# Kernel tuning notes

Measured on AMD Instinct MI355X. Metric: run time of the kernel, lower is better.

Reference implementation:

```python
import jax, jax.numpy as jnp
import numpy as np
from itertools import product

D = 64          # dense grid extent per axis
B = 2           # batch size
N_PER = 65536
NF_IN = 3
NF = 32
EPS = 1e-5


def _ravel(c):
    # c: [Q,4] (b,x,y,z) -> unique linear key
    return ((c[:, 0] * D + c[:, 1]) * D + c[:, 2]) * D + c[:, 3]


def _build_indices():
    """Build active coords and rule-book index tables (numpy, host-side)."""
    rng = np.random.default_rng(0)
    parts = []
    for b in range(B):
        lin = rng.choice(D ** 3, size=N_PER, replace=False)
        x = lin // (D * D)
        y = (lin // D) % D
        z = lin % D
        parts.append(np.stack([np.full(N_PER, b), x, y, z], 1))
    coords = np.concatenate(parts, 0).astype(np.int64)  # [N,4]
    keys = _ravel(coords)
    order = np.argsort(keys)
    skeys = keys[order]

    def lookup(qc):
        valid = ((qc[:, 1:] >= 0) & (qc[:, 1:] < D)).all(1)
        qc2 = np.where(valid[:, None], qc, 0)
        qk = _ravel(qc2)
        pos = np.clip(np.searchsorted(skeys, qk), 0, len(skeys) - 1)
        found = valid & (skeys[pos] == qk)
        return np.where(found, order[pos], -1)

    # 3x3x3 submanifold rule-book: neighbor index per active site per offset
    offs3 = list(product((-1, 0, 1), repeat=3))
    nbr = np.stack([lookup(coords + np.array([0, dx, dy, dz]))
                    for dx, dy, dz in offs3], 1)  # [N,27]
    # 2x2x2 stride-2 conv: output sites = unique parent cells
    parents = np.unique(np.concatenate([coords[:, :1], coords[:, 1:] // 2], 1), axis=0)
    base = parents * np.array([1, 2, 2, 2])
    offs2 = list(product((0, 1), repeat=3))
    child = np.stack([lookup(base + np.array([0, dx, dy, dz]))
                      for dx, dy, dz in offs2], 1)  # [M,8]
    return nbr.astype(np.int32), child.astype(np.int32)


def setup_inputs() -> dict:
    nbr, child = _build_indices()
    N = nbr.shape[0]
    key = jax.random.key(0)
    ks = jax.random.split(key, 6)

    def w(k, shape, fan):
        return jax.random.normal(k, shape, jnp.float32) / np.float32(np.sqrt(fan))

    ones = jnp.ones((NF,), jnp.float32)
    zeros = jnp.zeros((NF,), jnp.float32)
    return {
        "feats": jax.random.normal(ks[0], (N, NF_IN), jnp.float32),
        "nbr_idx": jnp.asarray(nbr),
        "child_idx": jnp.asarray(child),
        "W1": w(ks[1], (27, NF_IN, NF), 27 * NF_IN),
        "W2a": w(ks[2], (27, NF, NF), 27 * NF),
        "W2b": w(ks[3], (27, NF, NF), 27 * NF),
        "W3": w(ks[4], (8, NF, NF), 8 * NF),
        "g1": ones, "b1": zeros,
        "g2": ones, "b2": zeros,
        "g3": ones, "b3": zeros,
        "g4": ones, "b4": zeros,
    }


def _gconv(feats, idx, W):
    # sparse conv as rule-book gather -> per-offset GEMM -> accumulate
    mask = (idx >= 0)
    g = feats[jnp.clip(idx, 0)] * mask[..., None].astype(feats.dtype)  # [N,K,C]
    return jnp.einsum('nkc,kcd->nd', g, W)


def _bnrelu(x, g, b):
    # training-mode BN over active sites, then ReLU (scn.BatchNormReLU)
    mu = x.mean(0)
    var = x.var(0)
    return jax.nn.relu((x - mu) * jax.lax.rsqrt(var + EPS) * g + b)


def reference(feats, nbr_idx, child_idx, W1, W2a, W2b, W3,
              g1, b1, g2, b2, g3, b3, g4, b4):
    x1 = _gconv(feats, nbr_idx, W1)                       # p1: submanifold 3^3
    br = _gconv(_bnrelu(x1, g1, b1), nbr_idx, W2a)        # p2 residual branch
    br = _gconv(_bnrelu(br, g2, b2), nbr_idx, W2b)
    ft2 = _bnrelu(x1 + br, g3, b3)                        # AddTable + BNReLU
    x3 = _gconv(ft2, child_idx, W3)                       # p3: 2^3 stride-2 conv
    out = _bnrelu(x3, g4, b4)
    return (out, ft2)
```

## Files before the change

kernel.cpp:

```cpp
#include <hip/hip_runtime.h>
#include <hip/hip_bf16.h>


typedef __bf16 bf16_8 __attribute__((ext_vector_type(8)));
typedef float  f32x4  __attribute__((ext_vector_type(4)));

#define EPSV 1e-5f
#define NCOPY 32
#define CBLK 256

__global__ __launch_bounds__(256) void k_cnt(const int* __restrict__ child, int m8,
                                             int* __restrict__ blockCnt) {
    __shared__ int ws[4];
    const int b = blockIdx.x, tid = threadIdx.x;
    const int chunk = (m8 + CBLK - 1) / CBLK;
    const int s0 = b * chunk, s1 = min(s0 + chunk, m8);
    int c = 0;
    for (int s = s0 + tid; s < s1; s += 256) c += (child[s] >= 0);
#pragma unroll
    for (int d = 1; d < 64; d <<= 1) c += __shfl_xor(c, d);
    if ((tid & 63) == 0) ws[tid >> 6] = c;
    __syncthreads();
    if (tid == 0) blockCnt[b] = ws[0] + ws[1] + ws[2] + ws[3];
}

__global__ __launch_bounds__(256) void k_compact(const int* __restrict__ child, int m8,
                                                 const int* __restrict__ blockCnt,
                                                 int* __restrict__ perm,
                                                 int* __restrict__ invperm) {
    __shared__ int woff[4];
    __shared__ int sbase;
    const int b = blockIdx.x, tid = threadIdx.x;
    const int chunk = (m8 + CBLK - 1) / CBLK;
    const int s0 = b * chunk, s1 = min(s0 + chunk, m8);
    if (tid == 0) {
        int a = 0;
        for (int i = 0; i < b; ++i) a += blockCnt[i];
        sbase = a;
    }
    __syncthreads();
    int off = sbase;
    for (int base = s0; base < s1; base += 256) {
        const int s = base + tid;
        int c = -1;
        bool v = false;
        if (s < s1) { c = child[s]; v = (c >= 0); }
        unsigned long long m = __ballot(v);
        if ((tid & 63) == 0) woff[tid >> 6] = __popcll(m);
        __syncthreads();
        const int wv = tid >> 6;
        int wpre = 0;
#pragma unroll
        for (int i = 0; i < 4; ++i) if (i < wv) wpre += woff[i];
        const int tot = woff[0] + woff[1] + woff[2] + woff[3];
        const int rank = __popcll(m & ((1ULL << (tid & 63)) - 1ULL));
        if (v) {
            const int pos = off + wpre + rank;
            perm[pos] = c;
            invperm[c] = pos;
        }
        off += tot;
        __syncthreads();
    }
}

__global__ __launch_bounds__(256) void k_reindex(
    const int* __restrict__ nbr, const int* __restrict__ child,
    const int* __restrict__ perm, const int* __restrict__ invperm,
    const float* __restrict__ feats,
    const float* __restrict__ W1, const float* __restrict__ W2a,
    const float* __restrict__ W2b, const float* __restrict__ W3,
    int* __restrict__ nbrT, int* __restrict__ childT,
    __bf16* __restrict__ X, __bf16* __restrict__ T, __bf16* __restrict__ FB,
    __bf16* __restrict__ w1t, __bf16* __restrict__ w2at,
    __bf16* __restrict__ w2bt, __bf16* __restrict__ w3t,
    float* __restrict__ statsAll,
    int N, int M, int MP) {
    int t = blockIdx.x * 256 + threadIdx.x;
    if (t < 28 * N) {
        const int k = t / N, p = t - k * N;
        int o = N;
        if (k < 27) {
            const int v = nbr[(size_t)perm[p] * 27 + k];
            o = (v < 0) ? N : invperm[v];
        }
        nbrT[t] = o;
        return;
    }
    t -= 28 * N;
    if (t < 8 * MP) {
        const int k = t / MP, m = t - k * MP;
        int o = N;
        if (m < M) {
            const int v = child[(size_t)m * 8 + k];
            o = (v < 0) ? N : invperm[v];
        }
        childT[t] = o;
        return;
    }
    t -= 8 * MP;
    if (t < N * 32) {
        const int p = t >> 5, c = t & 31;
        FB[t] = (c < 3) ? (__bf16)feats[(size_t)perm[p] * 3 + c] : (__bf16)0.f;
        return;
    }
    t -= N * 32;
    if (t < 96) {
        const int b = t >> 5, c = t & 31;
        __bf16* p = (b == 0) ? X : (b == 1) ? T : FB;
        p[(size_t)N * 32 + c] = (__bf16)0.f;
        return;
    }
    t -= 96;
    if (t < 28672) {
        const int k = t >> 10, r = t & 1023, d = r >> 5, c = r & 31;
        w1t[t] = (k < 27 && c < 3) ? (__bf16)W1[(k * 3 + c) * 32 + d] : (__bf16)0.f;
        return;
    }
    t -= 28672;
    if (t < 28672) {
        const int k = t >> 10, r = t & 1023, d = r >> 5, c = r & 31;
        w2at[t] = (k < 27) ? (__bf16)W2a[(k * 32 + c) * 32 + d] : (__bf16)0.f;
        return;
    }
    t -= 28672;
    if (t < 28672) {
        const int k = t >> 10, r = t & 1023, d = r >> 5, c = r & 31;
        w2bt[t] = (k < 27) ? (__bf16)W2b[(k * 32 + c) * 32 + d] : (__bf16)0.f;
        return;
    }
    t -= 28672;
    if (t < 8192) {
        const int k = t >> 10, r = t & 1023, d = r >> 5, c = r & 31;
        w3t[t] = (__bf16)W3[(k * 32 + c) * 32 + d];
        return;
    }
    t -= 8192;
    if (t < 4 * NCOPY * 64) statsAll[t] = 0.f;
}

template <int KOFF, bool ADD>
__global__ __launch_bounds__(256, 4) void k_conv(
    const __bf16* __restrict__ src,
    const int* __restrict__ idxT,
    const __bf16* __restrict__ Wt,
    const __bf16* __restrict__ addsrc,
    __bf16* __restrict__ dst,
    float* __restrict__ spart_out,
    int nout, int npad) {
    constexpr int KPAD = ((KOFF + 3) / 4) * 4;
    constexpr int KPW = KPAD / 4;
    __shared__ float part[4][32][34];
    __shared__ float lst[64];

    const int tid = threadIdx.x;
    const int lane = tid & 63;
    const int wv = tid >> 6;
    const int base = blockIdx.x * 32;
    const int sl = lane & 15;
    const int kh = lane >> 4;
    const int kbeg = wv * KPW;

    if (tid < 64) lst[tid] = 0.f;

    int nb[2][KPW];
#pragma unroll
    for (int j = 0; j < KPW; ++j)
#pragma unroll
        for (int g = 0; g < 2; ++g)
            nb[g][j] = idxT[(kbeg + j) * npad + base + g * 16 + sl];

    bf16_8 av[2][KPW];
#pragma unroll
    for (int j = 0; j < KPW; ++j)
#pragma unroll
        for (int g = 0; g < 2; ++g)
            av[g][j] = *(const bf16_8*)(src + (size_t)nb[g][j] * 32 + kh * 8);
    __builtin_amdgcn_sched_barrier(0);

    f32x4 acc[2][2];
#pragma unroll
    for (int g = 0; g < 2; ++g)
#pragma unroll
        for (int h = 0; h < 2; ++h)
#pragma unroll
            for (int r = 0; r < 4; ++r) acc[g][h][r] = 0.f;

#pragma unroll
    for (int j = 0; j < KPW; ++j) {
        const int kk = kbeg + j;
        bf16_8 b0 = *(const bf16_8*)(Wt + kk * 1024 + sl * 32 + kh * 8);
        bf16_8 b1 = *(const bf16_8*)(Wt + kk * 1024 + (16 + sl) * 32 + kh * 8);
        acc[0][0] = __builtin_amdgcn_mfma_f32_16x16x32_bf16(av[0][j], b0, acc[0][0], 0, 0, 0);
        acc[0][1] = __builtin_amdgcn_mfma_f32_16x16x32_bf16(av[0][j], b1, acc[0][1], 0, 0, 0);
        acc[1][0] = __builtin_amdgcn_mfma_f32_16x16x32_bf16(av[1][j], b0, acc[1][0], 0, 0, 0);
        acc[1][1] = __builtin_amdgcn_mfma_f32_16x16x32_bf16(av[1][j], b1, acc[1][1], 0, 0, 0);
    }

#pragma unroll
    for (int g = 0; g < 2; ++g)
#pragma unroll
        for (int h = 0; h < 2; ++h)
#pragma unroll
            for (int r = 0; r < 4; ++r)
                part[wv][g * 16 + kh * 4 + r][h * 16 + sl] = acc[g][h][r];
    __syncthreads();

    if (tid < 128) {
        const int sloc = tid >> 2;
        const int c0 = (tid & 3) * 8;
        float v[8];
#pragma unroll
        for (int i = 0; i < 8; ++i)
            v[i] = part[0][sloc][c0 + i] + part[1][sloc][c0 + i] +
                   part[2][sloc][c0 + i] + part[3][sloc][c0 + i];
        const int site = base + sloc;
        if (site < nout) {
            if (ADD) {
                bf16_8 ad = *(const bf16_8*)(addsrc + (size_t)site * 32 + c0);
#pragma unroll
                for (int i = 0; i < 8; ++i) v[i] += (float)ad[i];
            }
            bf16_8 o;
#pragma unroll
            for (int i = 0; i < 8; ++i) o[i] = (__bf16)v[i];
            *(bf16_8*)(dst + (size_t)site * 32 + c0) = o;
        } else {
#pragma unroll
            for (int i = 0; i < 8; ++i) v[i] = 0.f;
        }
        float sv[8], qv[8];
#pragma unroll
        for (int i = 0; i < 8; ++i) { sv[i] = v[i]; qv[i] = v[i] * v[i]; }
#pragma unroll
        for (int d = 4; d < 64; d <<= 1) {
#pragma unroll
            for (int i = 0; i < 8; ++i) {
                sv[i] += __shfl_xor(sv[i], d);
                qv[i] += __shfl_xor(qv[i], d);
            }
        }
        if ((lane & 60) == 0) {
#pragma unroll
            for (int i = 0; i < 8; ++i) {
                atomicAdd(&lst[c0 + i], sv[i]);
                atomicAdd(&lst[32 + c0 + i], qv[i]);
            }
        }
    }
    __syncthreads();
    if (tid < 64)
        atomicAdd(&spart_out[(blockIdx.x & (NCOPY - 1)) * 64 + tid], lst[tid]);
}

template <bool WF32, bool WBF>
__global__ __launch_bounds__(256) void k_bn(
    const __bf16* __restrict__ src, const float* __restrict__ spart,
    const float* __restrict__ gamma, const float* __restrict__ beta,
    float inv_cnt, int nrows,
    __bf16* __restrict__ dstb, float* __restrict__ dstf,
    const int* __restrict__ permw) {
    __shared__ float ss[64];
    __shared__ float sc[32], sh[32];
    const int tid = threadIdx.x;
    if (tid < 64) {
        float a = 0.f;
#pragma unroll
        for (int i = 0; i < NCOPY; ++i) a += spart[i * 64 + tid];
        ss[tid] = a;
    }
    __syncthreads();
    if (tid < 32) {
        float mu = ss[tid] * inv_cnt;
        float var = ss[32 + tid] * inv_cnt - mu * mu;
        float s = gamma[tid] * rsqrtf(var + EPSV);
        sc[tid] = s;
        sh[tid] = beta[tid] - mu * s;
    }
    __syncthreads();
    const int gtid = blockIdx.x * blockDim.x + tid;
    const int c0 = (gtid & 3) * 8;
    float scale[8], shift[8];
#pragma unroll
    for (int i = 0; i < 8; ++i) { scale[i] = sc[c0 + i]; shift[i] = sh[c0 + i]; }
    const int rstride = (gridDim.x * blockDim.x) >> 2;
    for (int r = gtid >> 2; r < nrows; r += rstride) {
        const size_t off = (size_t)r * 32 + c0;
        bf16_8 v = *(const bf16_8*)(src + off);
        float y[8];
#pragma unroll
        for (int i = 0; i < 8; ++i) y[i] = fmaxf(fmaf((float)v[i], scale[i], shift[i]), 0.f);
        if (WBF) {
            bf16_8 o;
#pragma unroll
            for (int i = 0; i < 8; ++i) o[i] = (__bf16)y[i];
            *(bf16_8*)(dstb + off) = o;
        }
        if (WF32) {
            f32x4 lo, hi;
#pragma unroll
            for (int i = 0; i < 4; ++i) { lo[i] = y[i]; hi[i] = y[4 + i]; }
            const size_t woff = permw ? ((size_t)permw[r] * 32 + c0) : off;
            *(f32x4*)(dstf + woff) = lo;
            *(f32x4*)(dstf + woff + 4) = hi;
        }
    }
}

extern "C" void kernel_launch(void* const* d_in, const int* in_sizes, int n_in,
                              void* d_out, int out_size, void* d_ws, size_t ws_size,
                              hipStream_t stream) {
    const float* feats = (const float*)d_in[0];
    const int* nbr     = (const int*)d_in[1];
    const int* child   = (const int*)d_in[2];
    const float* W1  = (const float*)d_in[3];
    const float* W2a = (const float*)d_in[4];
    const float* W2b = (const float*)d_in[5];
    const float* W3  = (const float*)d_in[6];
    const float* g1 = (const float*)d_in[7];  const float* b1 = (const float*)d_in[8];
    const float* g2 = (const float*)d_in[9];  const float* b2 = (const float*)d_in[10];
    const float* g3 = (const float*)d_in[11]; const float* b3 = (const float*)d_in[12];
    const float* g4 = (const float*)d_in[13]; const float* b4 = (const float*)d_in[14];

    const int N = in_sizes[0] / 3;
    const int M8 = in_sizes[2];
    const int M = M8 / 8;
    const int MP = ((M + 31) / 32) * 32;

    float* outp = (float*)d_out;
    float* ft2p = outp + (size_t)M * 32;

    char* ws = (char*)d_ws;
    float* statsAll = (float*)ws;
    __bf16* w1t  = (__bf16*)(ws + 32768);
    __bf16* w2at = w1t + 28672;
    __bf16* w2bt = w2at + 28672;
    __bf16* w3t  = w2bt + 28672;
    __bf16* X  = (__bf16*)(ws + 221184);
    __bf16* T  = X + (size_t)(N + 1) * 32;
    __bf16* FB = T + (size_t)(N + 1) * 32;
    char* p2 = (char*)(FB + (size_t)(N + 1) * 32);
    int* perm    = (int*)p2;
    int* invperm = perm + N;
    int* nbrT    = invperm + N;
    int* childT  = nbrT + (size_t)28 * N;
    int* blockCnt = childT + (size_t)8 * MP;

    float* s1 = statsAll;
    float* s2 = statsAll + NCOPY * 64;
    float* s3 = statsAll + 2 * NCOPY * 64;
    float* s4 = statsAll + 3 * NCOPY * 64;

    k_cnt<<<CBLK, 256, 0, stream>>>(child, M8, blockCnt);
    k_compact<<<CBLK, 256, 0, stream>>>(child, M8, blockCnt, perm, invperm);

    const int rtot = 28 * N + 8 * MP + N * 32 + 96 + 3 * 28672 + 8192 + 4 * NCOPY * 64;
    k_reindex<<<(rtot + 255) / 256, 256, 0, stream>>>(
        nbr, child, perm, invperm, feats, W1, W2a, W2b, W3,
        nbrT, childT, X, T, FB, w1t, w2at, w2bt, w3t, statsAll, N, M, MP);

    const int cgrid = N / 32;
    const int cgrid3 = MP / 32;
    const float invN = 1.f / N, invM = 1.f / M;

    k_conv<27, false><<<cgrid, 256, 0, stream>>>(FB, nbrT, w1t, nullptr, X, s1, N, N);
    k_bn<false, true><<<1024, 256, 0, stream>>>(X, s1, g1, b1, invN, N, T, nullptr, nullptr);
    k_conv<27, false><<<cgrid, 256, 0, stream>>>(T, nbrT, w2at, nullptr, FB, s2, N, N);
    k_bn<false, true><<<1024, 256, 0, stream>>>(FB, s2, g2, b2, invN, N, T, nullptr, nullptr);
    k_conv<27, true><<<cgrid, 256, 0, stream>>>(T, nbrT, w2bt, X, FB, s3, N, N);
    k_bn<true, true><<<1024, 256, 0, stream>>>(FB, s3, g3, b3, invN, N, T, ft2p, perm);
    k_conv<8, false><<<cgrid3, 256, 0, stream>>>(T, childT, w3t, nullptr, X, s4, M, MP);
    k_bn<true, false><<<1024, 256, 0, stream>>>(X, s4, g4, b4, invM, M, nullptr, outp, nullptr);
}
```

Baseline: 181.2 us.

## Fuse BN-ReLU into submanifold convs via per-block deduplicated halo in LDS

A new k_halo kernel builds, for each 32-site block, a deduplicated list of up to 255 neighbour rows using a shared-memory hash table, plus byte-sized local indices. The three submanifold convs now stage these unique rows into LDS once, applying the previous layer's BN scale/shift and ReLU while loading. That removes two standalone k_bn passes and the redundant global gathers of shared neighbours. Rows that overflow the halo fall back to direct global loads. The cost is an extra hashing kernel, heavier LDS use that may limit occupancy, and the BN finalisation being repeated in every block.

Measured after the change: 199.2 us. +9.9%, slower.

```diff
diff --git a/kernel.cpp b/kernel.cpp
--- a/kernel.cpp
+++ b/kernel.cpp
@@ -8,6 +8,15 @@
 #define EPSV 1e-5f
 #define NCOPY 32
 #define CBLK 256
+#define HMAX 255
+#define HST 40
+
+__device__ inline bf16_8 bzero8() {
+    bf16_8 z;
+#pragma unroll
+    for (int i = 0; i < 8; ++i) z[i] = (__bf16)0.f;
+    return z;
+}
 
 __global__ __launch_bounds__(256) void k_cnt(const int* __restrict__ child, int m8,
                                              int* __restrict__ blockCnt) {
@@ -139,20 +148,233 @@
     if (t < 4 * NCOPY * 64) statsAll[t] = 0.f;
 }
 
-template <int KOFF, bool ADD>
-__global__ __launch_bounds__(256, 4) void k_conv(
+__global__ __launch_bounds__(256) void k_halo(
+    const int* __restrict__ nbrT, int N,
+    int* __restrict__ haloList, unsigned char* __restrict__ nbrL,
+    int* __restrict__ cntG) {
+    __shared__ int key[1024];
+    __shared__ int loc[1024];
+    __shared__ int hcnt;
+    const int b = blockIdx.x, tid = threadIdx.x;
+    const int base = b * 32;
+    for (int i = tid; i < 1024; i += 256) key[i] = -1;
+    if (tid == 0) hcnt = 0;
+    __syncthreads();
+    for (int e = tid; e < 896; e += 256) {
+        const int k = e >> 5, s = e & 31;
+        const int nb = nbrT[(size_t)k * N + base + s];
+        unsigned h = ((unsigned)nb * 2654435761u) >> 22;
+        while (true) {
+            int old = atomicCAS(&key[h], -1, nb);
+            if (old == -1 || old == nb) break;
+            h = (h + 1) & 1023;
+        }
+    }
+    __syncthreads();
+    for (int i = tid; i < 1024; i += 256) {
+        if (key[i] != -1) {
+            const int l = atomicAdd(&hcnt, 1);
+            if (l < HMAX) {
+                loc[i] = l;
+                haloList[(size_t)b * 256 + l] = key[i];
+            } else {
+                loc[i] = HMAX;
+            }
+        }
+    }
+    __syncthreads();
+    for (int e = tid; e < 896; e += 256) {
+        const int k = e >> 5, s = e & 31;
+        const int nb = nbrT[(size_t)k * N + base + s];
+        unsigned h = ((unsigned)nb * 2654435761u) >> 22;
+        while (key[h] != nb) h = (h + 1) & 1023;
+        nbrL[(size_t)b * 896 + e] = (unsigned char)loc[h];
+    }
+    if (tid == 0) cntG[b] = min(hcnt, HMAX);
+}
+
+template <bool ADD, bool BNST>
+__global__ __launch_bounds__(256, 4) void k_convh(
     const __bf16* __restrict__ src,
-    const int* __restrict__ idxT,
+    const int* __restrict__ nbrT,
+    const unsigned char* __restrict__ nbrL,
+    const int* __restrict__ haloList, const int* __restrict__ cntG,
     const __bf16* __restrict__ Wt,
     const __bf16* __restrict__ addsrc,
     __bf16* __restrict__ dst,
-    float* __restrict__ spart_out,
+    const float* __restrict__ spart_in,
+    const float* __restrict__ gamma, const float* __restrict__ beta,
+    float inv_cnt_in,
+    float* __restrict__ spart_out, int N) {
+    __shared__ __bf16 halo[HMAX * HST];
+    __shared__ float part[4][32][34];
+    __shared__ float lst[64];
+    __shared__ float sfin[64];
+    __shared__ float lsc[32], lsh[32];
+
+    const int tid = threadIdx.x;
+    const int lane = tid & 63;
+    const int wv = tid >> 6;
+    const int b = blockIdx.x;
+    const int base = b * 32;
+    const int sl = lane & 15;
+    const int kh = lane >> 4;
+    const int kbeg = wv * 7;
+
+    if (tid < 64) lst[tid] = 0.f;
+
+    if (BNST) {
+        if (tid < 64) {
+            float a = 0.f;
+#pragma unroll
+            for (int i = 0; i < NCOPY; ++i) a += spart_in[i * 64 + tid];
+            sfin[tid] = a;
+        }
+        __syncthreads();
+        if (tid < 32) {
+            float mu = sfin[tid] * inv_cnt_in;
+            float var = sfin[32 + tid] * inv_cnt_in - mu * mu;
+            float s = gamma[tid] * rsqrtf(var + EPSV);
+            lsc[tid] = s;
+            lsh[tid] = beta[tid] - mu * s;
+        }
+    }
+    __syncthreads();
+
+    const int cnt = cntG[b];
+    for (int i = tid; i < cnt * 4; i += 256) {
+        const int slot = i >> 2, q = i & 3;
+        const int row = haloList[(size_t)b * 256 + slot];
+        bf16_8 v = *(const bf16_8*)(src + (size_t)row * 32 + q * 8);
+        if (BNST) {
+            if (row == N) {
+                v = bzero8();
+            } else {
+#pragma unroll
+                for (int u = 0; u < 8; ++u)
+                    v[u] = (__bf16)fmaxf(fmaf((float)v[u], lsc[q * 8 + u], lsh[q * 8 + u]), 0.f);
+            }
+        }
+        *(bf16_8*)(&halo[slot * HST + q * 8]) = v;
+    }
+    __syncthreads();
+
+    unsigned char li[2][7];
+#pragma unroll
+    for (int j = 0; j < 7; ++j)
+#pragma unroll
+        for (int g = 0; g < 2; ++g)
+            li[g][j] = nbrL[(size_t)b * 896 + (kbeg + j) * 32 + g * 16 + sl];
+
+    bf16_8 av[2][7];
+#pragma unroll
+    for (int j = 0; j < 7; ++j)
+#pragma unroll
+        for (int g = 0; g < 2; ++g) {
+            const int la = li[g][j];
+            const int ls = (la == HMAX) ? 0 : la;
+            av[g][j] = *(const bf16_8*)(&halo[ls * HST + kh * 8]);
+        }
+#pragma unroll
+    for (int j = 0; j < 7; ++j)
+#pragma unroll
+        for (int g = 0; g < 2; ++g) {
+            if (li[g][j] == HMAX) {
+                const int row = nbrT[(size_t)(kbeg + j) * N + base + g * 16 + sl];
+                bf16_8 v = *(const bf16_8*)(src + (size_t)row * 32 + kh * 8);
+                if (BNST) {
+                    if (row == N) {
+                        v = bzero8();
+                    } else {
+#pragma unroll
+                        for (int u = 0; u < 8; ++u)
+                            v[u] = (__bf16)fmaxf(fmaf((float)v[u], lsc[kh * 8 + u], lsh[kh * 8 + u]), 0.f);
+                    }
+                }
+                av[g][j] = v;
+            }
+        }
+
+    f32x4 acc[2][2];
+#pragma unroll
+    for (int g = 0; g < 2; ++g)
+#pragma unroll
+        for (int h = 0; h < 2; ++h)
+#pragma unroll
+            for (int r = 0; r < 4; ++r) acc[g][h][r] = 0.f;
+
+#pragma unroll
+    for (int j = 0; j < 7; ++j) {
+        const int kk = kbeg + j;
+        bf16_8 b0 = *(const bf16_8*)(Wt + kk * 1024 + sl * 32 + kh * 8);
+        bf16_8 b1 = *(const bf16_8*)(Wt + kk * 1024 + (16 + sl) * 32 + kh * 8);
+        acc[0][0] = __builtin_amdgcn_mfma_f32_16x16x32_bf16(av[0][j], b0, acc[0][0], 0, 0, 0);
+        acc[0][1] = __builtin_amdgcn_mfma_f32_16x16x32_bf16(av[0][j], b1, acc[0][1], 0, 0, 0);
+        acc[1][0] = __builtin_amdgcn_mfma_f32_16x16x32_bf16(av[1][j], b0, acc[1][0], 0, 0, 0);
+        acc[1][1] = __builtin_amdgcn_mfma_f32_16x16x32_bf16(av[1][j], b1, acc[1][1], 0, 0, 0);
+    }
+
+#pragma unroll
+    for (int g = 0; g < 2; ++g)
+#pragma unroll
+        for (int h = 0; h < 2; ++h)
+#pragma unroll
+            for (int r = 0; r < 4; ++r)
+                part[wv][g * 16 + kh * 4 + r][h * 16 + sl] = acc[g][h][r];
+    __syncthreads();
+
+    if (tid < 128) {
+        const int sloc = tid >> 2;
+        const int c0 = (tid & 3) * 8;
+        float v[8];
+#pragma unroll
+        for (int i = 0; i < 8; ++i)
+            v[i] = part[0][sloc][c0 + i] + part[1][sloc][c0 + i] +
+                   part[2][sloc][c0 + i] + part[3][sloc][c0 + i];
+        const int site = base + sloc;
+        if (ADD) {
+            bf16_8 ad = *(const bf16_8*)(addsrc + (size_t)site * 32 + c0);
+#pragma unroll
+            for (int i = 0; i < 8; ++i) v[i] += (float)ad[i];
+        }
+        bf16_8 o;
+#pragma unroll
+        for (int i = 0; i < 8; ++i) o[i] = (__bf16)v[i];
+        *(bf16_8*)(dst + (size_t)site * 32 + c0) = o;
+        float sv[8], qv[8];
+#pragma unroll
+        for (int i = 0; i < 8; ++i) { sv[i] = v[i]; qv[i] = v[i] * v[i]; }
+#pragma unroll
+        for (int d = 4; d < 64; d <<= 1) {
+#pragma unroll
+            for (int i = 0; i < 8; ++i) {
+                sv[i] += __shfl_xor(sv[i], d);
+                qv[i] += __shfl_xor(qv[i], d);
+            }
+        }
+        if ((lane & 60) == 0) {
+#pragma unroll
+            for (int i = 0; i < 8; ++i) {
+                atomicAdd(&lst[c0 + i], sv[i]);
+                atomicAdd(&lst[32 + c0 + i], qv[i]);
+            }
+        }
+    }
+    __syncthreads();
+    if (tid < 64)
+        atomicAdd(&spart_out[(b & (NCOPY - 1)) * 64 + tid], lst[tid]);
+}
+
+template <int KOFF, bool ADD>
+__global__ __launch_bounds__(256, 4) void k_conv(
+    const __bf16* __restrict__ src, const int* __restrict__ idxT,
+    const __bf16* __restrict__ Wt, const __bf16* __restrict__ addsrc,
+    __bf16* __restrict__ dst, float* __restrict__ spart_out,
     int nout, int npad) {
     constexpr int KPAD = ((KOFF + 3) / 4) * 4;
     constexpr int KPW = KPAD / 4;
     __shared__ float part[4][32][34];
     __shared__ float lst[64];
-
     const int tid = threadIdx.x;
     const int lane = tid & 63;
     const int wv = tid >> 6;
@@ -160,24 +382,19 @@
     const int sl = lane & 15;
     const int kh = lane >> 4;
     const int kbeg = wv * KPW;
-
     if (tid < 64) lst[tid] = 0.f;
-
     int nb[2][KPW];
 #pragma unroll
     for (int j = 0; j < KPW; ++j)
 #pragma unroll
         for (int g = 0; g < 2; ++g)
             nb[g][j] = idxT[(kbeg + j) * npad + base + g * 16 + sl];
-
     bf16_8 av[2][KPW];
 #pragma unroll
     for (int j = 0; j < KPW; ++j)
 #pragma unroll
         for (int g = 0; g < 2; ++g)
             av[g][j] = *(const bf16_8*)(src + (size_t)nb[g][j] * 32 + kh * 8);
-    __builtin_amdgcn_sched_barrier(0);
-
     f32x4 acc[2][2];
 #pragma unroll
     for (int g = 0; g < 2; ++g)
@@ -185,7 +402,6 @@
         for (int h = 0; h < 2; ++h)
 #pragma unroll
             for (int r = 0; r < 4; ++r) acc[g][h][r] = 0.f;
-
 #pragma unroll
     for (int j = 0; j < KPW; ++j) {
         const int kk = kbeg + j;
@@ -196,7 +412,6 @@
         acc[1][0] = __builtin_amdgcn_mfma_f32_16x16x32_bf16(av[1][j], b0, acc[1][0], 0, 0, 0);
         acc[1][1] = __builtin_amdgcn_mfma_f32_16x16x32_bf16(av[1][j], b1, acc[1][1], 0, 0, 0);
     }
-
 #pragma unroll
     for (int g = 0; g < 2; ++g)
 #pragma unroll
@@ -205,7 +420,6 @@
             for (int r = 0; r < 4; ++r)
                 part[wv][g * 16 + kh * 4 + r][h * 16 + sl] = acc[g][h][r];
     __syncthreads();
-
     if (tid < 128) {
         const int sloc = tid >> 2;
         const int c0 = (tid & 3) * 8;
@@ -326,6 +540,7 @@
     const int M8 = in_sizes[2];
     const int M = M8 / 8;
     const int MP = ((M + 31) / 32) * 32;
+    const int NB = N / 32;
 
     float* outp = (float*)d_out;
     float* ft2p = outp + (size_t)M * 32;
@@ -345,6 +560,9 @@
     int* nbrT    = invperm + N;
     int* childT  = nbrT + (size_t)28 * N;
     int* blockCnt = childT + (size_t)8 * MP;
+    int* haloList = blockCnt + 256;
+    int* cntG     = haloList + (size_t)NB * 256;
+    unsigned char* nbrL = (unsigned char*)(cntG + NB);
 
     float* s1 = statsAll;
     float* s2 = statsAll + NCOPY * 64;
@@ -359,16 +577,20 @@
         nbr, child, perm, invperm, feats, W1, W2a, W2b, W3,
         nbrT, childT, X, T, FB, w1t, w2at, w2bt, w3t, statsAll, N, M, MP);
 
-    const int cgrid = N / 32;
-    const int cgrid3 = MP / 32;
+    k_halo<<<NB, 256, 0, stream>>>(nbrT, N, haloList, nbrL, cntG);
+
     const float invN = 1.f / N, invM = 1.f / M;
 
-    k_conv<27, false><<<cgrid, 256, 0, stream>>>(FB, nbrT, w1t, nullptr, X, s1, N, N);
-    k_bn<false, true><<<1024, 256, 0, stream>>>(X, s1, g1, b1, invN, N, T, nullptr, nullptr);
-    k_conv<27, false><<<cgrid, 256, 0, stream>>>(T, nbrT, w2at, nullptr, FB, s2, N, N);
-    k_bn<false, true><<<1024, 256, 0, stream>>>(FB, s2, g2, b2, invN, N, T, nullptr, nullptr);
-    k_conv<27, true><<<cgrid, 256, 0, stream>>>(T, nbrT, w2bt, X, FB, s3, N, N);
+    k_convh<false, false><<<NB, 256, 0, stream>>>(
+        FB, nbrT, nbrL, haloList, cntG, w1t, nullptr, X,
+        nullptr, nullptr, nullptr, 0.f, s1, N);
+    k_convh<false, true><<<NB, 256, 0, stream>>>(
+        X, nbrT, nbrL, haloList, cntG, w2at, nullptr, T,
+        s1, g1, b1, invN, s2, N);
+    k_convh<true, true><<<NB, 256, 0, stream>>>(
+        T, nbrT, nbrL, haloList, cntG, w2bt, X, FB,
+        s2, g2, b2, invN, s3, N);
     k_bn<true, true><<<1024, 256, 0, stream>>>(FB, s3, g3, b3, invN, N, T, ft2p, perm);
-    k_conv<8, false><<<cgrid3, 256, 0, stream>>>(T, childT, w3t, nullptr, X, s4, M, MP);
+    k_conv<8, false><<<MP / 32, 256, 0, stream>>>(T, childT, w3t, nullptr, X, s4, M, MP);
     k_bn<true, false><<<1024, 256, 0, stream>>>(X, s4, g4, b4, invM, M, nullptr, outp, nullptr);
 }
```
